# Performance work log

Hardware: AMD Instinct MI355X
Metric: run time of the kernel (lower is better)

## Reference

```python
import jax, jax.numpy as jnp
import numpy as np

N_NODES = 100000
N_EDGES = 1600000
IN_DIM, HID_DIM, OUT_DIM = 128, 128, 64


def setup_inputs() -> dict:
    key = jax.random.key(0)
    k1, k2, k3, k4, k5, k6, k7 = jax.random.split(key, 7)
    in_feat = jax.random.normal(k1, (N_NODES, IN_DIM), dtype=jnp.float32)
    src = jax.random.randint(k2, (N_EDGES,), 0, N_NODES, dtype=jnp.int32)
    dst = jax.random.randint(k3, (N_EDGES,), 0, N_NODES, dtype=jnp.int32)
    # GraphConv params (Glorot-style scale)
    W1 = jax.random.normal(k4, (IN_DIM, HID_DIM), dtype=jnp.float32) * (2.0 / (IN_DIM + HID_DIM)) ** 0.5
    b1 = jnp.zeros((HID_DIM,), dtype=jnp.float32)
    W2 = jax.random.normal(k5, (HID_DIM, OUT_DIM), dtype=jnp.float32) * (2.0 / (HID_DIM + OUT_DIM)) ** 0.5
    b2 = jnp.zeros((OUT_DIM,), dtype=jnp.float32)
    return {"in_feat": in_feat, "W1": W1, "b1": b1, "W2": W2, "b2": b2, "src": src, "dst": dst}


def _graph_conv(x, W, b, src, dst, inv_sqrt_out, inv_sqrt_in):
    # DGL GraphConv, norm='both': D_out^{-1/2} on source, sum-aggregate, D_in^{-1/2} on dest
    x = x * inv_sqrt_out[:, None]              # [N, d]
    msg = x[src]                               # gather: [E, d]
    agg = jax.ops.segment_sum(msg, dst, num_segments=x.shape[0])  # scatter-add: [N, d]
    agg = agg * inv_sqrt_in[:, None]
    return agg @ W + b


def reference(in_feat, W1, b1, W2, b2, src, dst):
    N = in_feat.shape[0]
    ones = jnp.ones(src.shape[0], dtype=in_feat.dtype)
    deg_out = jax.ops.segment_sum(ones, src, num_segments=N)
    deg_in = jax.ops.segment_sum(ones, dst, num_segments=N)
    # clamp degree to >= 1 (DGL behavior) before inverse sqrt
    inv_sqrt_out = jnp.maximum(deg_out, 1.0) ** -0.5
    inv_sqrt_in = jnp.maximum(deg_in, 1.0) ** -0.5
    h = _graph_conv(in_feat, W1, b1, src, dst, inv_sqrt_out, inv_sqrt_in)
    h = jax.nn.relu(h)
    h = _graph_conv(h, W2, b2, src, dst, inv_sqrt_out, inv_sqrt_in)
    return h
```

## Files before the change

kernel.cpp:

```cpp
#include <hip/hip_runtime.h>

#define N_NODES 100000
#define N_EDGES 1600000
#define IN_DIM 128
#define HID_DIM 128
#define OUT_DIM 64

#define NB 391
#define GRIDB 256
#define EPB (N_EDGES / GRIDB)

typedef unsigned short ushort_t;
typedef unsigned int uint_t;
typedef unsigned char uchar_t;
typedef __attribute__((ext_vector_type(8))) short bf16x8;
typedef __attribute__((ext_vector_type(4))) float f32x4;

__device__ __forceinline__ float blo(uint_t u) { return __uint_as_float(u << 16); }
__device__ __forceinline__ float bhi(uint_t u) { return __uint_as_float(u & 0xFFFF0000u); }
__device__ __forceinline__ uint_t f2b(float f) {
    uint_t u = __float_as_uint(f);
    uint_t r = u + 0x7FFFu + ((u >> 16) & 1u);
    return r >> 16;
}
__device__ __forceinline__ uint_t pk2(float a, float b) { return f2b(a) | (f2b(b) << 16); }


__global__ __launch_bounds__(256) void histdeg_k(const int* __restrict__ src,
                                                 const int* __restrict__ dst,
                                                 int* __restrict__ bucketTot,
                                                 int* __restrict__ bucketTotS) {
    __shared__ int hd[NB];
    __shared__ int hs[NB];
    int t = threadIdx.x, blk = blockIdx.x;
    for (int j = t; j < NB; j += 256) { hd[j] = 0; hs[j] = 0; }
    __syncthreads();
    int e0 = blk * EPB;
    for (int i = e0 + t; i < e0 + EPB; i += 256) {
        atomicAdd(&hd[dst[i] >> 8], 1);
        atomicAdd(&hs[src[i] >> 8], 1);
    }
    __syncthreads();
    for (int j = t; j < NB; j += 256) {
        if (hd[j]) atomicAdd(&bucketTot[j], hd[j]);
        if (hs[j]) atomicAdd(&bucketTotS[j], hs[j]);
    }
}


__global__ __launch_bounds__(512) void bscan_k(const int* __restrict__ bucketTot,
                                               const int* __restrict__ bucketTotS,
                                               int* __restrict__ bucketOfs,
                                               int* __restrict__ fill,
                                               int* __restrict__ bucketOfsS,
                                               int* __restrict__ fillS) {
    __shared__ int s[512];
    int t = threadIdx.x;
    int v = (t < NB) ? bucketTot[t] : 0;
    s[t] = v;
    __syncthreads();
    for (int off = 1; off < 512; off <<= 1) {
        int x = (t >= off) ? s[t - off] : 0;
        __syncthreads();
        s[t] += x;
        __syncthreads();
    }
    if (t < NB) {
        int e = s[t] - v;
        bucketOfs[t] = e;
        fill[t] = e;
    }
    if (t == 0) bucketOfs[NB] = N_EDGES;
    __syncthreads();
    int v2 = (t < NB) ? bucketTotS[t] : 0;
    s[t] = v2;
    __syncthreads();
    for (int off = 1; off < 512; off <<= 1) {
        int x = (t >= off) ? s[t - off] : 0;
        __syncthreads();
        s[t] += x;
        __syncthreads();
    }
    if (t < NB) {
        int e = s[t] - v2;
        bucketOfsS[t] = e;
        fillS[t] = e;
    }
    if (t == 0) bucketOfsS[NB] = N_EDGES;
}


__global__ __launch_bounds__(256) void scat_k(const int* __restrict__ src,
                                              const int* __restrict__ dst,
                                              int* __restrict__ fill,
                                              int* __restrict__ fillS,
                                              uint_t* __restrict__ ebuf,
                                              uchar_t* __restrict__ sbuf) {
    __shared__ int lcnt[NB];
    __shared__ int base[NB];
    __shared__ int lpos[NB];
    __shared__ int lcntS[NB];
    __shared__ int baseS[NB];
    __shared__ int lposS[NB];
    int t = threadIdx.x, blk = blockIdx.x;
    for (int j = t; j < NB; j += 256) {
        lcnt[j] = 0; lpos[j] = 0; lcntS[j] = 0; lposS[j] = 0;
    }
    __syncthreads();
    int e0 = blk * EPB;
    for (int i = e0 + t; i < e0 + EPB; i += 256) {
        atomicAdd(&lcnt[dst[i] >> 8], 1);
        atomicAdd(&lcntS[src[i] >> 8], 1);
    }
    __syncthreads();
    for (int j = t; j < NB; j += 256) {
        int c = lcnt[j];
        base[j] = c ? atomicAdd(&fill[j], c) : 0;
        int cs = lcntS[j];
        baseS[j] = cs ? atomicAdd(&fillS[j], cs) : 0;
    }
    __syncthreads();
    for (int i = e0 + t; i < e0 + EPB; i += 256) {
        int sv = src[i], d = dst[i];
        int b = d >> 8;
        int slot = atomicAdd(&lpos[b], 1);
        ebuf[base[b] + slot] = (uint_t)sv | ((uint_t)(d & 255) << 17);
        int bs = sv >> 8;
        int slotS = atomicAdd(&lposS[bs], 1);
        sbuf[baseS[bs] + slotS] = (uchar_t)(sv & 255);
    }
}


__global__ __launch_bounds__(256) void finx_k(const uint_t* __restrict__ ebuf,
                                              const uchar_t* __restrict__ sbuf,
                                              const int* __restrict__ bucketOfs,
                                              const int* __restrict__ bucketOfsS,
                                              int* __restrict__ ofs,
                                              int* __restrict__ esrc,
                                              int* __restrict__ dego) {
    __shared__ int cnt[256];
    __shared__ int s[256];
    __shared__ int fil[256];
    int t = threadIdx.x;
    int blk = blockIdx.x;

    if (blk >= NB) {
        int b = blk - NB;
        int e0 = bucketOfsS[b], e1 = bucketOfsS[b + 1];
        cnt[t] = 0;
        __syncthreads();
        for (int i = e0 + t; i < e1; i += 256) atomicAdd(&cnt[sbuf[i]], 1);
        __syncthreads();
        int node = b * 256 + t;
        if (node < N_NODES) dego[node] = cnt[t];
        return;
    }

    int b = blk;
    int e0 = bucketOfs[b], e1 = bucketOfs[b + 1];
    cnt[t] = 0;
    __syncthreads();
    for (int i = e0 + t; i < e1; i += 256) atomicAdd(&cnt[ebuf[i] >> 17], 1);
    __syncthreads();
    int c = cnt[t];
    s[t] = c;
    __syncthreads();
    for (int off = 1; off < 256; off <<= 1) {
        int x = (t >= off) ? s[t - off] : 0;
        __syncthreads();
        s[t] += x;
        __syncthreads();
    }
    int excl = s[t] - c;
    int node = b * 256 + t;
    if (node < N_NODES) ofs[node] = e0 + excl;
    if (b == NB - 1 && t == 0) ofs[N_NODES] = N_EDGES;
    fil[t] = excl;
    __syncthreads();
    for (int i = e0 + t; i < e1; i += 256) {
        uint_t u = ebuf[i];
        int slot = atomicAdd(&fil[u >> 17], 1);
        esrc[e0 + slot] = (int)(u & 0x1FFFFu);
    }
}


__global__ __launch_bounds__(256) void prepw_k(const float* __restrict__ x,
                                               const int* __restrict__ dego,
                                               ushort_t* __restrict__ xs,
                                               const float* __restrict__ W1,
                                               const float* __restrict__ W2,
                                               ushort_t* __restrict__ Wf1,
                                               ushort_t* __restrict__ Wf2) {
    constexpr int NB_PREP = N_NODES * 16 / 256;
    if ((int)blockIdx.x < NB_PREP) {
        int gid = blockIdx.x * 256 + threadIdx.x;
        int row = gid >> 4;
        float s = rsqrtf(fmaxf((float)dego[row], 1.0f));
        const float4* xp = (const float4*)x + (size_t)gid * 2;
        float4 va = xp[0], vb = xp[1];
        ((uint4*)xs)[gid] = make_uint4(pk2(va.x * s, va.y * s), pk2(va.z * s, va.w * s),
                                       pk2(vb.x * s, vb.y * s), pk2(vb.z * s, vb.w * s));
        return;
    }
    int gid = (blockIdx.x - NB_PREP) * 256 + threadIdx.x;
    const float* W;
    ushort_t* Wf;
    int BN;
    if (gid < HID_DIM * 16) {
        W = W1; Wf = Wf1; BN = HID_DIM;
    } else {
        gid -= HID_DIM * 16;
        if (gid >= OUT_DIM * 16) return;
        W = W2; Wf = Wf2; BN = OUT_DIM;
    }
    int l = gid & 63;
    int kc = (gid >> 6) & 3;
    int nt = gid >> 8;
    int col = nt * 16 + (l & 15);
    int k0 = kc * 32 + (l >> 4) * 8;
    uint_t r[4];
    #pragma unroll
    for (int p = 0; p < 4; ++p)
        r[p] = pk2(W[(size_t)(k0 + 2 * p) * BN + col], W[(size_t)(k0 + 2 * p + 1) * BN + col]);
    ((uint4*)Wf)[gid] = make_uint4(r[0], r[1], r[2], r[3]);
}

#define ACC8(v)                                         \
    acc[0] += blo(v.x); acc[1] += bhi(v.x);             \
    acc[2] += blo(v.y); acc[3] += bhi(v.y);             \
    acc[4] += blo(v.z); acc[5] += bhi(v.z);             \
    acc[6] += blo(v.w); acc[7] += bhi(v.w);


__global__ __launch_bounds__(256) void agg128_k(const ushort_t* __restrict__ xs,
                                                const int* __restrict__ esrc,
                                                const int* __restrict__ ofs,
                                                ushort_t* __restrict__ a) {
    int wid = (blockIdx.x * 256 + threadIdx.x) >> 6;
    int lane = threadIdx.x & 63;
    int q = lane >> 4, li = lane & 15;
    int beg = ofs[wid], end = ofs[wid + 1];
    float acc[8];
    #pragma unroll
    for (int i = 0; i < 8; ++i) acc[i] = 0.f;

    for (int j = beg; j < end; j += 64) {
        int m = end - j;
        if (m > 64) m = 64;
        int idx = (lane < m) ? esrc[j + lane] : 0;
        for (int t = 0; 4 * t < m; t += 4) {
            int e0 = 4 * t + q, e1 = e0 + 4, e2 = e0 + 8, e3 = e0 + 12;
            int s0 = __shfl(idx, e0 & 63);
            int s1 = __shfl(idx, e1 & 63);
            int s2 = __shfl(idx, e2 & 63);
            int s3 = __shfl(idx, e3 & 63);
            uint4 v0 = *(const uint4*)(xs + (size_t)s0 * 128 + li * 8);
            uint4 v1 = *(const uint4*)(xs + (size_t)s1 * 128 + li * 8);
            uint4 v2 = *(const uint4*)(xs + (size_t)s2 * 128 + li * 8);
            uint4 v3 = *(const uint4*)(xs + (size_t)s3 * 128 + li * 8);
            if (e0 < m) { ACC8(v0) }
            if (e1 < m) { ACC8(v1) }
            if (e2 < m) { ACC8(v2) }
            if (e3 < m) { ACC8(v3) }
        }
    }
    #pragma unroll
    for (int i = 0; i < 8; ++i) acc[i] += __shfl(acc[i], lane ^ 16);
    #pragma unroll
    for (int i = 0; i < 8; ++i) acc[i] += __shfl(acc[i], lane ^ 32);

    if (lane < 16) {
        float sc = rsqrtf(fmaxf((float)(end - beg), 1.0f));
        *(uint4*)(a + (size_t)wid * 128 + li * 8) =
            make_uint4(pk2(acc[0] * sc, acc[1] * sc), pk2(acc[2] * sc, acc[3] * sc),
                       pk2(acc[4] * sc, acc[5] * sc), pk2(acc[6] * sc, acc[7] * sc));
    }
}


__global__ __launch_bounds__(256) void mgemm12_k(const ushort_t* __restrict__ A,
                                                 const ushort_t* __restrict__ Wf1,
                                                 const ushort_t* __restrict__ Wf2,
                                                 const float* __restrict__ b1,
                                                 const int* __restrict__ dego,
                                                 ushort_t* __restrict__ ys) {
    __shared__ ushort_t Hs[4][16][136];
    int wv = threadIdx.x >> 6;
    int l = threadIdx.x & 63;
    int r0 = (blockIdx.x * 4 + wv) * 16;
    if (r0 >= N_NODES) return;
    int q = l >> 4, li = l & 15;

    const ushort_t* ap = A + (size_t)(r0 + li) * 128 + q * 8;
    bf16x8 af[4];
    #pragma unroll
    for (int kc = 0; kc < 4; ++kc) af[kc] = *(const bf16x8*)(ap + kc * 32);

    f32x4 acc[8];
    #pragma unroll
    for (int nt = 0; nt < 8; ++nt) acc[nt] = (f32x4){0.f, 0.f, 0.f, 0.f};

    #pragma unroll
    for (int kc = 0; kc < 4; ++kc) {
        #pragma unroll
        for (int nt = 0; nt < 8; ++nt) {
            bf16x8 bfr = *(const bf16x8*)(Wf1 + ((size_t)(nt * 4 + kc) * 64 + l) * 8);
            acc[nt] = __builtin_amdgcn_mfma_f32_16x16x32_bf16(af[kc], bfr, acc[nt], 0, 0, 0);
        }
    }

    #pragma unroll
    for (int nt = 0; nt < 8; ++nt) {
        float bv = b1[nt * 16 + li];
        #pragma unroll
        for (int j = 0; j < 4; ++j) {
            float x = fmaxf(acc[nt][j] + bv, 0.0f);
            Hs[wv][q * 4 + j][nt * 16 + li] = (ushort_t)f2b(x);
        }
    }

    bf16x8 hf[4];
    #pragma unroll
    for (int kc = 0; kc < 4; ++kc)
        hf[kc] = *(const bf16x8*)&Hs[wv][li][kc * 32 + q * 8];

    f32x4 acc2[4];
    #pragma unroll
    for (int nt = 0; nt < 4; ++nt) acc2[nt] = (f32x4){0.f, 0.f, 0.f, 0.f};

    #pragma unroll
    for (int kc = 0; kc < 4; ++kc) {
        #pragma unroll
        for (int nt = 0; nt < 4; ++nt) {
            bf16x8 bfr = *(const bf16x8*)(Wf2 + ((size_t)(nt * 4 + kc) * 64 + l) * 8);
            acc2[nt] = __builtin_amdgcn_mfma_f32_16x16x32_bf16(hf[kc], bfr, acc2[nt], 0, 0, 0);
        }
    }

    int orow = r0 + q * 4;
    float os[4];
    #pragma unroll
    for (int j = 0; j < 4; ++j) os[j] = rsqrtf(fmaxf((float)dego[orow + j], 1.0f));
    #pragma unroll
    for (int nt = 0; nt < 4; ++nt) {
        #pragma unroll
        for (int j = 0; j < 4; ++j) {
            ys[(size_t)(orow + j) * 64 + nt * 16 + li] = (ushort_t)f2b(acc2[nt][j] * os[j]);
        }
    }
}


__global__ __launch_bounds__(256) void agg64_k(const ushort_t* __restrict__ ys,
                                               const int* __restrict__ esrc,
                                               const int* __restrict__ ofs,
                                               const float* __restrict__ b2,
                                               float* __restrict__ out) {
    int wid = (blockIdx.x * 256 + threadIdx.x) >> 6;
    int lane = threadIdx.x & 63;
    int og = lane >> 3, li = lane & 7;
    int beg = ofs[wid], end = ofs[wid + 1];
    float acc[8];
    #pragma unroll
    for (int i = 0; i < 8; ++i) acc[i] = 0.f;

    for (int j = beg; j < end; j += 64) {
        int m = end - j;
        if (m > 64) m = 64;
        int idx = (lane < m) ? esrc[j + lane] : 0;
        for (int t = 0; 8 * t < m; t += 2) {
            int e0 = 8 * t + og, e1 = e0 + 8;
            int s0 = __shfl(idx, e0 & 63);
            int s1 = __shfl(idx, e1 & 63);
            uint4 v0 = *(const uint4*)(ys + (size_t)s0 * 64 + li * 8);
            uint4 v1 = *(const uint4*)(ys + (size_t)s1 * 64 + li * 8);
            if (e0 < m) { ACC8(v0) }
            if (e1 < m) { ACC8(v1) }
        }
    }
    #pragma unroll
    for (int i = 0; i < 8; ++i) acc[i] += __shfl(acc[i], lane ^ 8);
    #pragma unroll
    for (int i = 0; i < 8; ++i) acc[i] += __shfl(acc[i], lane ^ 16);
    #pragma unroll
    for (int i = 0; i < 8; ++i) acc[i] += __shfl(acc[i], lane ^ 32);

    if (lane < 8) {
        float sc = rsqrtf(fmaxf((float)(end - beg), 1.0f));
        float4 ba = *(const float4*)(b2 + li * 8);
        float4 bb = *(const float4*)(b2 + li * 8 + 4);
        float* op = out + (size_t)wid * 64 + li * 8;
        *(float4*)op = make_float4(acc[0] * sc + ba.x, acc[1] * sc + ba.y,
                                   acc[2] * sc + ba.z, acc[3] * sc + ba.w);
        *(float4*)(op + 4) = make_float4(acc[4] * sc + bb.x, acc[5] * sc + bb.y,
                                         acc[6] * sc + bb.z, acc[7] * sc + bb.w);
    }
}

extern "C" void kernel_launch(void* const* d_in, const int* in_sizes, int n_in,
                              void* d_out, int out_size, void* d_ws, size_t ws_size,
                              hipStream_t stream) {
    const float* in_feat = (const float*)d_in[0];
    const float* W1 = (const float*)d_in[1];
    const float* b1 = (const float*)d_in[2];
    const float* W2 = (const float*)d_in[3];
    const float* b2 = (const float*)d_in[4];
    const int* src = (const int*)d_in[5];
    const int* dst = (const int*)d_in[6];
    float* out = (float*)d_out;

    char* w = (char*)d_ws;
    int* bucketTot = (int*)w;   w += 392 * 4;
    int* bucketTotS = (int*)w;  w += 392 * 4;
    int* fill = (int*)w;        w += 392 * 4;
    int* fillS = (int*)w;       w += 392 * 4;
    int* bucketOfs = (int*)w;   w += 400 * 4;
    int* bucketOfsS = (int*)w;  w += 400 * 4;
    int* dego = (int*)w;        w += (size_t)(N_NODES + 8) * 4;
    int* ofs = (int*)w;         w += (size_t)(N_NODES + 8) * 4;
    uint_t* ebuf = (uint_t*)w;  w += (size_t)N_EDGES * 4;
    int* esrc = (int*)w;        w += (size_t)N_EDGES * 4;
    uchar_t* sbuf = (uchar_t*)w; w += (size_t)N_EDGES;
    w += (16 - ((size_t)w & 15)) & 15;
    ushort_t* Wf1 = (ushort_t*)w; w += (size_t)HID_DIM * 16 * 16;
    ushort_t* Wf2 = (ushort_t*)w; w += (size_t)OUT_DIM * 16 * 16;
    ushort_t* bufA = (ushort_t*)w; w += (size_t)N_NODES * HID_DIM * 2;
    ushort_t* bufB = (ushort_t*)w; w += (size_t)N_NODES * HID_DIM * 2;

    hipMemsetAsync(bucketTot, 0, 2 * 392 * 4, stream);

    histdeg_k<<<GRIDB, 256, 0, stream>>>(src, dst, bucketTot, bucketTotS);
    bscan_k<<<1, 512, 0, stream>>>(bucketTot, bucketTotS, bucketOfs, fill, bucketOfsS, fillS);
    scat_k<<<GRIDB, 256, 0, stream>>>(src, dst, fill, fillS, ebuf, sbuf);
    finx_k<<<2 * NB, 256, 0, stream>>>(ebuf, sbuf, bucketOfs, bucketOfsS, ofs, esrc, dego);

    prepw_k<<<N_NODES * 16 / 256 + 12, 256, 0, stream>>>(in_feat, dego, bufA, W1, W2, Wf1, Wf2);

    agg128_k<<<N_NODES / 4, 256, 0, stream>>>(bufA, esrc, ofs, bufB);

    mgemm12_k<<<(N_NODES / 16 + 3) / 4, 256, 0, stream>>>(bufB, Wf1, Wf2, b1, dego, bufA);

    agg64_k<<<N_NODES / 4, 256, 0, stream>>>(bufA, esrc, ofs, b2, out);
}
```

Measured before the change: 231.8 us.

## Fuse CSR build kernels into one cooperative kernel with grid syncs

The memset plus the four CSR construction kernels (histogram, bucket scan, scatter, per-bucket finalize) become a single cooperative launch of 782 blocks, separated by grid-wide barriers. The histogram pass now spreads its edges over all 782 blocks, and both bucket scans run in parallel on two blocks using a double-buffered scan. The goal is to remove launch gaps and the overhead of a separate memset. In exchange there are four grid syncs, a larger shared-memory footprint per block, and the requirement that all 782 blocks be co-resident.

```diff
diff --git a/kernel.cpp b/kernel.cpp
--- a/kernel.cpp
+++ b/kernel.cpp
@@ -1,4 +1,7 @@
 #include <hip/hip_runtime.h>
+#include <hip/hip_cooperative_groups.h>
+
+namespace cg = cooperative_groups;
 
 #define N_NODES 100000
 #define N_EDGES 1600000
@@ -9,6 +12,8 @@
 #define NB 391
 #define GRIDB 256
 #define EPB (N_EDGES / GRIDB)
+#define GRIDC (2 * NB)
+#define EPBH ((N_EDGES + GRIDC - 1) / GRIDC)
 
 typedef unsigned short ushort_t;
 typedef unsigned int uint_t;
@@ -26,162 +31,145 @@
 __device__ __forceinline__ uint_t pk2(float a, float b) { return f2b(a) | (f2b(b) << 16); }
 
 
-__global__ __launch_bounds__(256) void histdeg_k(const int* __restrict__ src,
-                                                 const int* __restrict__ dst,
-                                                 int* __restrict__ bucketTot,
-                                                 int* __restrict__ bucketTotS) {
-    __shared__ int hd[NB];
-    __shared__ int hs[NB];
+__global__ __launch_bounds__(256) void csr_coop_k(
+    const int* __restrict__ src, const int* __restrict__ dst,
+    int* __restrict__ bucketTot, int* __restrict__ bucketTotS,
+    int* __restrict__ bucketOfs, int* __restrict__ bucketOfsS,
+    int* __restrict__ fill, int* __restrict__ fillS,
+    uint_t* __restrict__ ebuf, uchar_t* __restrict__ sbuf,
+    int* __restrict__ ofs, int* __restrict__ esrc, int* __restrict__ dego) {
+    cg::grid_group grid = cg::this_grid();
+    __shared__ int sm[2400];
     int t = threadIdx.x, blk = blockIdx.x;
-    for (int j = t; j < NB; j += 256) { hd[j] = 0; hs[j] = 0; }
-    __syncthreads();
-    int e0 = blk * EPB;
-    for (int i = e0 + t; i < e0 + EPB; i += 256) {
-        atomicAdd(&hd[dst[i] >> 8], 1);
-        atomicAdd(&hs[src[i] >> 8], 1);
-    }
-    __syncthreads();
-    for (int j = t; j < NB; j += 256) {
-        if (hd[j]) atomicAdd(&bucketTot[j], hd[j]);
-        if (hs[j]) atomicAdd(&bucketTotS[j], hs[j]);
-    }
-}
-
-
-__global__ __launch_bounds__(512) void bscan_k(const int* __restrict__ bucketTot,
-                                               const int* __restrict__ bucketTotS,
-                                               int* __restrict__ bucketOfs,
-                                               int* __restrict__ fill,
-                                               int* __restrict__ bucketOfsS,
-                                               int* __restrict__ fillS) {
-    __shared__ int s[512];
-    int t = threadIdx.x;
-    int v = (t < NB) ? bucketTot[t] : 0;
-    s[t] = v;
-    __syncthreads();
-    for (int off = 1; off < 512; off <<= 1) {
-        int x = (t >= off) ? s[t - off] : 0;
-        __syncthreads();
-        s[t] += x;
-        __syncthreads();
-    }
-    if (t < NB) {
-        int e = s[t] - v;
-        bucketOfs[t] = e;
-        fill[t] = e;
-    }
-    if (t == 0) bucketOfs[NB] = N_EDGES;
-    __syncthreads();
-    int v2 = (t < NB) ? bucketTotS[t] : 0;
-    s[t] = v2;
-    __syncthreads();
-    for (int off = 1; off < 512; off <<= 1) {
-        int x = (t >= off) ? s[t - off] : 0;
-        __syncthreads();
-        s[t] += x;
-        __syncthreads();
-    }
-    if (t < NB) {
-        int e = s[t] - v2;
-        bucketOfsS[t] = e;
-        fillS[t] = e;
-    }
-    if (t == 0) bucketOfsS[NB] = N_EDGES;
-}
-
-
-__global__ __launch_bounds__(256) void scat_k(const int* __restrict__ src,
-                                              const int* __restrict__ dst,
-                                              int* __restrict__ fill,
-                                              int* __restrict__ fillS,
-                                              uint_t* __restrict__ ebuf,
-                                              uchar_t* __restrict__ sbuf) {
-    __shared__ int lcnt[NB];
-    __shared__ int base[NB];
-    __shared__ int lpos[NB];
-    __shared__ int lcntS[NB];
-    __shared__ int baseS[NB];
-    __shared__ int lposS[NB];
-    int t = threadIdx.x, blk = blockIdx.x;
-    for (int j = t; j < NB; j += 256) {
-        lcnt[j] = 0; lpos[j] = 0; lcntS[j] = 0; lposS[j] = 0;
-    }
-    __syncthreads();
-    int e0 = blk * EPB;
-    for (int i = e0 + t; i < e0 + EPB; i += 256) {
-        atomicAdd(&lcnt[dst[i] >> 8], 1);
-        atomicAdd(&lcntS[src[i] >> 8], 1);
-    }
-    __syncthreads();
-    for (int j = t; j < NB; j += 256) {
-        int c = lcnt[j];
-        base[j] = c ? atomicAdd(&fill[j], c) : 0;
-        int cs = lcntS[j];
-        baseS[j] = cs ? atomicAdd(&fillS[j], cs) : 0;
-    }
-    __syncthreads();
-    for (int i = e0 + t; i < e0 + EPB; i += 256) {
-        int sv = src[i], d = dst[i];
-        int b = d >> 8;
-        int slot = atomicAdd(&lpos[b], 1);
-        ebuf[base[b] + slot] = (uint_t)sv | ((uint_t)(d & 255) << 17);
-        int bs = sv >> 8;
-        int slotS = atomicAdd(&lposS[bs], 1);
-        sbuf[baseS[bs] + slotS] = (uchar_t)(sv & 255);
-    }
-}
-
-
-__global__ __launch_bounds__(256) void finx_k(const uint_t* __restrict__ ebuf,
-                                              const uchar_t* __restrict__ sbuf,
-                                              const int* __restrict__ bucketOfs,
-                                              const int* __restrict__ bucketOfsS,
-                                              int* __restrict__ ofs,
-                                              int* __restrict__ esrc,
-                                              int* __restrict__ dego) {
-    __shared__ int cnt[256];
-    __shared__ int s[256];
-    __shared__ int fil[256];
-    int t = threadIdx.x;
-    int blk = blockIdx.x;
-
-    if (blk >= NB) {
-        int b = blk - NB;
-        int e0 = bucketOfsS[b], e1 = bucketOfsS[b + 1];
-        cnt[t] = 0;
-        __syncthreads();
-        for (int i = e0 + t; i < e1; i += 256) atomicAdd(&cnt[sbuf[i]], 1);
-        __syncthreads();
-        int node = b * 256 + t;
-        if (node < N_NODES) dego[node] = cnt[t];
-        return;
-    }
-
-    int b = blk;
-    int e0 = bucketOfs[b], e1 = bucketOfs[b + 1];
-    cnt[t] = 0;
-    __syncthreads();
-    for (int i = e0 + t; i < e1; i += 256) atomicAdd(&cnt[ebuf[i] >> 17], 1);
-    __syncthreads();
-    int c = cnt[t];
-    s[t] = c;
-    __syncthreads();
-    for (int off = 1; off < 256; off <<= 1) {
-        int x = (t >= off) ? s[t - off] : 0;
-        __syncthreads();
-        s[t] += x;
-        __syncthreads();
-    }
-    int excl = s[t] - c;
-    int node = b * 256 + t;
-    if (node < N_NODES) ofs[node] = e0 + excl;
-    if (b == NB - 1 && t == 0) ofs[N_NODES] = N_EDGES;
-    fil[t] = excl;
-    __syncthreads();
-    for (int i = e0 + t; i < e1; i += 256) {
-        uint_t u = ebuf[i];
-        int slot = atomicAdd(&fil[u >> 17], 1);
-        esrc[e0 + slot] = (int)(u & 0x1FFFFu);
+
+    {
+        int g = blk * 256 + t;
+        if (g < 392) bucketTot[g] = 0;
+        else if (g < 784) bucketTotS[g - 392] = 0;
+    }
+    grid.sync();
+
+    {
+        int* hd = sm;
+        int* hs = sm + 400;
+        for (int j = t; j < NB; j += 256) { hd[j] = 0; hs[j] = 0; }
+        __syncthreads();
+        int e0 = blk * EPBH;
+        int e1 = e0 + EPBH;
+        if (e1 > N_EDGES) e1 = N_EDGES;
+        for (int i = e0 + t; i < e1; i += 256) {
+            atomicAdd(&hd[dst[i] >> 8], 1);
+            atomicAdd(&hs[src[i] >> 8], 1);
+        }
+        __syncthreads();
+        for (int j = t; j < NB; j += 256) {
+            if (hd[j]) atomicAdd(&bucketTot[j], hd[j]);
+            if (hs[j]) atomicAdd(&bucketTotS[j], hs[j]);
+        }
+    }
+    grid.sync();
+
+    if (blk < 2) {
+        const int* tot = (blk == 0) ? bucketTot : bucketTotS;
+        int* bofs = (blk == 0) ? bucketOfs : bucketOfsS;
+        int* fl = (blk == 0) ? fill : fillS;
+        int* a = sm;
+        int* b = sm + 512;
+        a[t] = (t < NB) ? tot[t] : 0;
+        a[t + 256] = (t + 256 < NB) ? tot[t + 256] : 0;
+        __syncthreads();
+        for (int off = 1; off < 512; off <<= 1) {
+            b[t] = a[t] + ((t >= off) ? a[t - off] : 0);
+            b[t + 256] = a[t + 256] + ((t + 256 >= off) ? a[t + 256 - off] : 0);
+            __syncthreads();
+            int* tmp = a; a = b; b = tmp;
+        }
+        for (int idx = t; idx < NB; idx += 256) {
+            int e = a[idx] - tot[idx];
+            bofs[idx] = e;
+            fl[idx] = e;
+        }
+        if (t == 0) bofs[NB] = N_EDGES;
+    }
+    grid.sync();
+
+    if (blk < GRIDB) {
+        int* lcnt = sm;
+        int* base = sm + 400;
+        int* lpos = sm + 800;
+        int* lcntS = sm + 1200;
+        int* baseS = sm + 1600;
+        int* lposS = sm + 2000;
+        for (int j = t; j < NB; j += 256) {
+            lcnt[j] = 0; lpos[j] = 0; lcntS[j] = 0; lposS[j] = 0;
+        }
+        __syncthreads();
+        int e0 = blk * EPB;
+        for (int i = e0 + t; i < e0 + EPB; i += 256) {
+            atomicAdd(&lcnt[dst[i] >> 8], 1);
+            atomicAdd(&lcntS[src[i] >> 8], 1);
+        }
+        __syncthreads();
+        for (int j = t; j < NB; j += 256) {
+            int c = lcnt[j];
+            base[j] = c ? atomicAdd(&fill[j], c) : 0;
+            int cs = lcntS[j];
+            baseS[j] = cs ? atomicAdd(&fillS[j], cs) : 0;
+        }
+        __syncthreads();
+        for (int i = e0 + t; i < e0 + EPB; i += 256) {
+            int sv = src[i], d = dst[i];
+            int b = d >> 8;
+            int slot = atomicAdd(&lpos[b], 1);
+            ebuf[base[b] + slot] = (uint_t)sv | ((uint_t)(d & 255) << 17);
+            int bs = sv >> 8;
+            int slotS = atomicAdd(&lposS[bs], 1);
+            sbuf[baseS[bs] + slotS] = (uchar_t)(sv & 255);
+        }
+    }
+    grid.sync();
+
+    {
+        int* cnt = sm;
+        int* s = sm + 256;
+        int* fil = sm + 512;
+        if (blk >= NB) {
+            int b = blk - NB;
+            int e0 = bucketOfsS[b], e1 = bucketOfsS[b + 1];
+            cnt[t] = 0;
+            __syncthreads();
+            for (int i = e0 + t; i < e1; i += 256) atomicAdd(&cnt[sbuf[i]], 1);
+            __syncthreads();
+            int node = b * 256 + t;
+            if (node < N_NODES) dego[node] = cnt[t];
+        } else {
+            int b = blk;
+            int e0 = bucketOfs[b], e1 = bucketOfs[b + 1];
+            cnt[t] = 0;
+            __syncthreads();
+            for (int i = e0 + t; i < e1; i += 256) atomicAdd(&cnt[ebuf[i] >> 17], 1);
+            __syncthreads();
+            int c = cnt[t];
+            s[t] = c;
+            __syncthreads();
+            for (int off = 1; off < 256; off <<= 1) {
+                int x = (t >= off) ? s[t - off] : 0;
+                __syncthreads();
+                s[t] += x;
+                __syncthreads();
+            }
+            int excl = s[t] - c;
+            int node = b * 256 + t;
+            if (node < N_NODES) ofs[node] = e0 + excl;
+            if (b == NB - 1 && t == 0) ofs[N_NODES] = N_EDGES;
+            fil[t] = excl;
+            __syncthreads();
+            for (int i = e0 + t; i < e1; i += 256) {
+                uint_t u = ebuf[i];
+                int slot = atomicAdd(&fil[u >> 17], 1);
+                esrc[e0 + slot] = (int)(u & 0x1FFFFu);
+            }
+        }
     }
 }
 
@@ -429,12 +417,10 @@
     ushort_t* bufA = (ushort_t*)w; w += (size_t)N_NODES * HID_DIM * 2;
     ushort_t* bufB = (ushort_t*)w; w += (size_t)N_NODES * HID_DIM * 2;
 
-    hipMemsetAsync(bucketTot, 0, 2 * 392 * 4, stream);
-
-    histdeg_k<<<GRIDB, 256, 0, stream>>>(src, dst, bucketTot, bucketTotS);
-    bscan_k<<<1, 512, 0, stream>>>(bucketTot, bucketTotS, bucketOfs, fill, bucketOfsS, fillS);
-    scat_k<<<GRIDB, 256, 0, stream>>>(src, dst, fill, fillS, ebuf, sbuf);
-    finx_k<<<2 * NB, 256, 0, stream>>>(ebuf, sbuf, bucketOfs, bucketOfsS, ofs, esrc, dego);
+    void* cargs[] = {(void*)&src, (void*)&dst, (void*)&bucketTot, (void*)&bucketTotS,
+                     (void*)&bucketOfs, (void*)&bucketOfsS, (void*)&fill, (void*)&fillS,
+                     (void*)&ebuf, (void*)&sbuf, (void*)&ofs, (void*)&esrc, (void*)&dego};
+    hipLaunchCooperativeKernel((void*)csr_coop_k, dim3(GRIDC), dim3(256), cargs, 0, stream);
 
     prepw_k<<<N_NODES * 16 / 256 + 12, 256, 0, stream>>>(in_feat, dego, bufA, W1, W2, Wf1, Wf2);
 
```

Measured after the change: 537.1 us. 2.32x slower.

## Reuse per-block histograms in scatter and fuse feature prep into finx kernel

Applied to the files above, without the earlier changes.

histdeg_k now writes its per-block bucket counts to global memory, and scat_k reads them back instead of making a second histogram pass over src/dst. The separate prepw_k launch is removed. Its feature scaling and bf16 conversion moves into the source-degree blocks of finx_k, using the shared-memory counts directly, and its weight packing moves into extra finx_k blocks. This saves one kernel launch and one full read of the edge arrays, at the cost of a small histogram buffer and heavier finx_k blocks that each convert 256 rows.

```diff
diff --git a/kernel.cpp b/kernel.cpp
--- a/kernel.cpp
+++ b/kernel.cpp
@@ -9,6 +9,7 @@
 #define NB 391
 #define GRIDB 256
 #define EPB (N_EDGES / GRIDB)
+#define HSTRIDE 400
 
 typedef unsigned short ushort_t;
 typedef unsigned int uint_t;
@@ -29,7 +30,9 @@
 __global__ __launch_bounds__(256) void histdeg_k(const int* __restrict__ src,
                                                  const int* __restrict__ dst,
                                                  int* __restrict__ bucketTot,
-                                                 int* __restrict__ bucketTotS) {
+                                                 int* __restrict__ bucketTotS,
+                                                 int* __restrict__ hist,
+                                                 int* __restrict__ histS) {
     __shared__ int hd[NB];
     __shared__ int hs[NB];
     int t = threadIdx.x, blk = blockIdx.x;
@@ -42,8 +45,11 @@
     }
     __syncthreads();
     for (int j = t; j < NB; j += 256) {
-        if (hd[j]) atomicAdd(&bucketTot[j], hd[j]);
-        if (hs[j]) atomicAdd(&bucketTotS[j], hs[j]);
+        int d = hd[j], s = hs[j];
+        hist[blk * HSTRIDE + j] = d;
+        histS[blk * HSTRIDE + j] = s;
+        if (d) atomicAdd(&bucketTot[j], d);
+        if (s) atomicAdd(&bucketTotS[j], s);
     }
 }
 
@@ -92,34 +98,27 @@
 
 __global__ __launch_bounds__(256) void scat_k(const int* __restrict__ src,
                                               const int* __restrict__ dst,
+                                              const int* __restrict__ hist,
+                                              const int* __restrict__ histS,
                                               int* __restrict__ fill,
                                               int* __restrict__ fillS,
                                               uint_t* __restrict__ ebuf,
                                               uchar_t* __restrict__ sbuf) {
-    __shared__ int lcnt[NB];
     __shared__ int base[NB];
     __shared__ int lpos[NB];
-    __shared__ int lcntS[NB];
     __shared__ int baseS[NB];
     __shared__ int lposS[NB];
     int t = threadIdx.x, blk = blockIdx.x;
     for (int j = t; j < NB; j += 256) {
-        lcnt[j] = 0; lpos[j] = 0; lcntS[j] = 0; lposS[j] = 0;
+        int c = hist[blk * HSTRIDE + j];
+        base[j] = c ? atomicAdd(&fill[j], c) : 0;
+        lpos[j] = 0;
+        int cs = histS[blk * HSTRIDE + j];
+        baseS[j] = cs ? atomicAdd(&fillS[j], cs) : 0;
+        lposS[j] = 0;
     }
     __syncthreads();
     int e0 = blk * EPB;
-    for (int i = e0 + t; i < e0 + EPB; i += 256) {
-        atomicAdd(&lcnt[dst[i] >> 8], 1);
-        atomicAdd(&lcntS[src[i] >> 8], 1);
-    }
-    __syncthreads();
-    for (int j = t; j < NB; j += 256) {
-        int c = lcnt[j];
-        base[j] = c ? atomicAdd(&fill[j], c) : 0;
-        int cs = lcntS[j];
-        baseS[j] = cs ? atomicAdd(&fillS[j], cs) : 0;
-    }
-    __syncthreads();
     for (int i = e0 + t; i < e0 + EPB; i += 256) {
         int sv = src[i], d = dst[i];
         int b = d >> 8;
@@ -138,13 +137,46 @@
                                               const int* __restrict__ bucketOfsS,
                                               int* __restrict__ ofs,
                                               int* __restrict__ esrc,
-                                              int* __restrict__ dego) {
+                                              int* __restrict__ dego,
+                                              const float* __restrict__ x,
+                                              ushort_t* __restrict__ xs,
+                                              const float* __restrict__ W1,
+                                              const float* __restrict__ W2,
+                                              ushort_t* __restrict__ Wf1,
+                                              ushort_t* __restrict__ Wf2) {
     __shared__ int cnt[256];
     __shared__ int s[256];
     __shared__ int fil[256];
     int t = threadIdx.x;
     int blk = blockIdx.x;
 
+    if (blk >= 2 * NB) {
+        int gid = (blk - 2 * NB) * 256 + t;
+        const float* W;
+        ushort_t* Wf;
+        int BN;
+        if (gid < HID_DIM * 16) {
+            W = W1; Wf = Wf1; BN = HID_DIM;
+        } else {
+            gid -= HID_DIM * 16;
+            if (gid >= OUT_DIM * 16) return;
+            W = W2; Wf = Wf2; BN = OUT_DIM;
+        }
+        int l = gid & 63;
+        int kc = (gid >> 6) & 3;
+        int nt = gid >> 8;
+        int col = nt * 16 + (l & 15);
+        int k0 = kc * 32 + (l >> 4) * 8;
+        uint_t r[4];
+        #pragma unroll
+        for (int p = 0; p < 4; ++p)
+            r[p] = pk2(W[(size_t)(k0 + 2 * p) * BN + col], W[(size_t)(k0 + 2 * p + 1) * BN + col]);
+        ((uint4*)Wf)[((blk - 2 * NB) * 256 + t < HID_DIM * 16) ? (blk - 2 * NB) * 256 + t
+                                                               : (blk - 2 * NB) * 256 + t - HID_DIM * 16] =
+            make_uint4(r[0], r[1], r[2], r[3]);
+        return;
+    }
+
     if (blk >= NB) {
         int b = blk - NB;
         int e0 = bucketOfsS[b], e1 = bucketOfsS[b + 1];
@@ -154,6 +186,20 @@
         __syncthreads();
         int node = b * 256 + t;
         if (node < N_NODES) dego[node] = cnt[t];
+        int nrows = N_NODES - b * 256;
+        if (nrows > 256) nrows = 256;
+        int chunks = nrows * 16;
+        for (int c = t; c < chunks; c += 256) {
+            int lrow = c >> 4;
+            int sub = c & 15;
+            int row = b * 256 + lrow;
+            float sc = rsqrtf(fmaxf((float)cnt[lrow], 1.0f));
+            const float4* xp = (const float4*)(x + (size_t)row * 128 + sub * 8);
+            float4 va = xp[0], vb = xp[1];
+            *(uint4*)(xs + (size_t)row * 128 + sub * 8) =
+                make_uint4(pk2(va.x * sc, va.y * sc), pk2(va.z * sc, va.w * sc),
+                           pk2(vb.x * sc, vb.y * sc), pk2(vb.z * sc, vb.w * sc));
+        }
         return;
     }
 
@@ -167,9 +213,9 @@
     s[t] = c;
     __syncthreads();
     for (int off = 1; off < 256; off <<= 1) {
-        int x = (t >= off) ? s[t - off] : 0;
-        __syncthreads();
-        s[t] += x;
+        int x2 = (t >= off) ? s[t - off] : 0;
+        __syncthreads();
+        s[t] += x2;
         __syncthreads();
     }
     int excl = s[t] - c;
@@ -183,48 +229,6 @@
         int slot = atomicAdd(&fil[u >> 17], 1);
         esrc[e0 + slot] = (int)(u & 0x1FFFFu);
     }
-}
-
-
-__global__ __launch_bounds__(256) void prepw_k(const float* __restrict__ x,
-                                               const int* __restrict__ dego,
-                                               ushort_t* __restrict__ xs,
-                                               const float* __restrict__ W1,
-                                               const float* __restrict__ W2,
-                                               ushort_t* __restrict__ Wf1,
-                                               ushort_t* __restrict__ Wf2) {
-    constexpr int NB_PREP = N_NODES * 16 / 256;
-    if ((int)blockIdx.x < NB_PREP) {
-        int gid = blockIdx.x * 256 + threadIdx.x;
-        int row = gid >> 4;
-        float s = rsqrtf(fmaxf((float)dego[row], 1.0f));
-        const float4* xp = (const float4*)x + (size_t)gid * 2;
-        float4 va = xp[0], vb = xp[1];
-        ((uint4*)xs)[gid] = make_uint4(pk2(va.x * s, va.y * s), pk2(va.z * s, va.w * s),
-                                       pk2(vb.x * s, vb.y * s), pk2(vb.z * s, vb.w * s));
-        return;
-    }
-    int gid = (blockIdx.x - NB_PREP) * 256 + threadIdx.x;
-    const float* W;
-    ushort_t* Wf;
-    int BN;
-    if (gid < HID_DIM * 16) {
-        W = W1; Wf = Wf1; BN = HID_DIM;
-    } else {
-        gid -= HID_DIM * 16;
-        if (gid >= OUT_DIM * 16) return;
-        W = W2; Wf = Wf2; BN = OUT_DIM;
-    }
-    int l = gid & 63;
-    int kc = (gid >> 6) & 3;
-    int nt = gid >> 8;
-    int col = nt * 16 + (l & 15);
-    int k0 = kc * 32 + (l >> 4) * 8;
-    uint_t r[4];
-    #pragma unroll
-    for (int p = 0; p < 4; ++p)
-        r[p] = pk2(W[(size_t)(k0 + 2 * p) * BN + col], W[(size_t)(k0 + 2 * p + 1) * BN + col]);
-    ((uint4*)Wf)[gid] = make_uint4(r[0], r[1], r[2], r[3]);
 }
 
 #define ACC8(v)                                         \
@@ -418,6 +422,8 @@
     int* fillS = (int*)w;       w += 392 * 4;
     int* bucketOfs = (int*)w;   w += 400 * 4;
     int* bucketOfsS = (int*)w;  w += 400 * 4;
+    int* hist = (int*)w;        w += (size_t)GRIDB * HSTRIDE * 4;
+    int* histS = (int*)w;       w += (size_t)GRIDB * HSTRIDE * 4;
     int* dego = (int*)w;        w += (size_t)(N_NODES + 8) * 4;
     int* ofs = (int*)w;         w += (size_t)(N_NODES + 8) * 4;
     uint_t* ebuf = (uint_t*)w;  w += (size_t)N_EDGES * 4;
@@ -431,12 +437,11 @@
 
     hipMemsetAsync(bucketTot, 0, 2 * 392 * 4, stream);
 
-    histdeg_k<<<GRIDB, 256, 0, stream>>>(src, dst, bucketTot, bucketTotS);
+    histdeg_k<<<GRIDB, 256, 0, stream>>>(src, dst, bucketTot, bucketTotS, hist, histS);
     bscan_k<<<1, 512, 0, stream>>>(bucketTot, bucketTotS, bucketOfs, fill, bucketOfsS, fillS);
-    scat_k<<<GRIDB, 256, 0, stream>>>(src, dst, fill, fillS, ebuf, sbuf);
-    finx_k<<<2 * NB, 256, 0, stream>>>(ebuf, sbuf, bucketOfs, bucketOfsS, ofs, esrc, dego);
-
-    prepw_k<<<N_NODES * 16 / 256 + 12, 256, 0, stream>>>(in_feat, dego, bufA, W1, W2, Wf1, Wf2);
+    scat_k<<<GRIDB, 256, 0, stream>>>(src, dst, hist, histS, fill, fillS, ebuf, sbuf);
+    finx_k<<<2 * NB + 12, 256, 0, stream>>>(ebuf, sbuf, bucketOfs, bucketOfsS, ofs, esrc, dego,
+                                            in_feat, bufA, W1, W2, Wf1, Wf2);
 
     agg128_k<<<N_NODES / 4, 256, 0, stream>>>(bufA, esrc, ofs, bufB);
 
```

Measured after the change: 223.7 us. -3.5%, faster.
